# Performance work log

Measured on AMD Instinct MI355X. Metric: run time of the kernel, lower is better.

## Reference

```python
import jax, jax.numpy as jnp
import numpy as np

D_MODEL = 1024
NHEAD = 16
HEAD_DIM = D_MODEL // NHEAD


def setup_inputs() -> dict:
    key = jax.random.key(0)
    ks = jax.random.split(key, 11)
    B, L, D = 4, 2048, D_MODEL
    s = 1.0 / np.sqrt(D)  # ~ torch Linear init scale
    return {
        "queries": jax.random.normal(ks[0], (B, L, D), jnp.float32),
        "keys": jax.random.normal(ks[1], (B, L, D), jnp.float32),
        "values": jax.random.normal(ks[2], (B, L, D), jnp.float32),
        "Wq": jax.random.normal(ks[3], (D, D), jnp.float32) * s,
        "bq": jnp.zeros((D,), jnp.float32),
        "Wk": jax.random.normal(ks[4], (D, D), jnp.float32) * s,
        "bk": jnp.zeros((D,), jnp.float32),
        "Wv": jax.random.normal(ks[5], (D, D), jnp.float32) * s,
        "bv": jnp.zeros((D,), jnp.float32),
        "Wo": jax.random.normal(ks[6], (D, D), jnp.float32) * s,
        "bo": jnp.zeros((D,), jnp.float32),
    }


def reference(queries, keys, values, Wq, bq, Wk, bk, Wv, bv, Wo, bo):
    B, L, D = queries.shape
    H, dh = NHEAD, HEAD_DIM
    # projections (W stored as [in, out])
    q = (queries @ Wq + bq).reshape(B, L, H, dh).transpose(0, 2, 1, 3)  # [B,H,L,dh]
    k = (keys @ Wk + bk).reshape(B, L, H, dh).transpose(0, 2, 1, 3)
    v = (values @ Wv + bv).reshape(B, L, H, dh).transpose(0, 2, 1, 3)
    scores = jnp.einsum("bhqd,bhkd->bhqk", q, k) / jnp.sqrt(jnp.float32(dh))
    attn = jax.nn.softmax(scores, axis=-1)  # dropout p=0 -> identity
    ctx = jnp.einsum("bhqk,bhkd->bhqd", attn, v)
    ctx = ctx.transpose(0, 2, 1, 3).reshape(B, L, D)
    return ctx @ Wo + bo
```

## Files before the change

### kernel.cpp

```cpp
#include <hip/hip_runtime.h>
#include <math.h>


using f32x4 = __attribute__((ext_vector_type(4))) float;
using bf16x8 = __attribute__((ext_vector_type(8))) short;

__device__ __forceinline__ unsigned short f2bf(float x) {
  union { float f; unsigned u; } v; v.f = x;
  unsigned r = v.u + 0x7fff + ((v.u >> 16) & 1);
  return (unsigned short)(r >> 16);
}

__device__ __forceinline__ void g2l16(const void* g, void* l) {
  __builtin_amdgcn_global_load_lds(
      (const __attribute__((address_space(1))) unsigned int*)g,
      (__attribute__((address_space(3))) unsigned int*)l, 16, 0, 0);
}

__global__ __launch_bounds__(256) void wt_k(const float* __restrict__ W,
                                            short* __restrict__ hiT) {
  __shared__ float t[64][65];
  const int n0 = blockIdx.x * 64, k0 = blockIdx.y * 64;
  const int tid = threadIdx.x;
  const int r = tid >> 4, c4 = (tid & 15) * 4;
#pragma unroll
  for (int i = 0; i < 4; i++) {
    const int row = r + i * 16;
    const float4 v = *(const float4*)&W[(size_t)(k0 + row) * 1024 + n0 + c4];
    t[c4 + 0][row] = v.x;
    t[c4 + 1][row] = v.y;
    t[c4 + 2][row] = v.z;
    t[c4 + 3][row] = v.w;
  }
  __syncthreads();
#pragma unroll
  for (int i = 0; i < 4; i++) {
    const int row = r + i * 16;
    short4 h;
    h.x = (short)f2bf(t[row][c4 + 0]);
    h.y = (short)f2bf(t[row][c4 + 1]);
    h.z = (short)f2bf(t[row][c4 + 2]);
    h.w = (short)f2bf(t[row][c4 + 3]);
    *(short4*)&hiT[(size_t)(n0 + row) * 1024 + k0 + c4] = h;
  }
}

template <int AFP32, int EPI>
__global__ __launch_bounds__(256, 2) void gemm_mfma_k(
    const void* __restrict__ A_g, const short* __restrict__ B_g,
    const float* __restrict__ bias, void* __restrict__ out0) {
  __shared__ short smem[64 * 144];
  short* As = smem;
  short* Bs = smem + 4096;

  const int tid = threadIdx.x;
  const int lane = tid & 63;
  const int wave = tid >> 6;
  const int quad = lane >> 4;
  const int l16 = lane & 15;
  const int m0 = blockIdx.x * 128;
  const int n0 = blockIdx.y * 128;
  const int wm = (wave >> 1) * 64;
  const int wn = (wave & 1) * 64;

  const int srow = tid >> 2;
  const int soff = (tid & 3) * 8;
  const int arow = tid >> 1;
  const int acol = (tid & 1) * 16;

  f32x4 acc[4][4];
#pragma unroll
  for (int i = 0; i < 4; i++)
#pragma unroll
    for (int j = 0; j < 4; j++) acc[i][j] = f32x4{0.f, 0.f, 0.f, 0.f};

  float4 apre[4];
  if (AFP32) {
    const float* Af = (const float*)A_g;
#pragma unroll
    for (int j = 0; j < 4; j++)
      apre[j] = *(const float4*)&Af[(size_t)(m0 + arow) * 1024 + acol + j * 4];
  }

  for (int k0 = 0; k0 < 1024; k0 += 32) {
    __syncthreads();
    if (AFP32) {
      short tmp[16];
      const float af[16] = {apre[0].x, apre[0].y, apre[0].z, apre[0].w,
                            apre[1].x, apre[1].y, apre[1].z, apre[1].w,
                            apre[2].x, apre[2].y, apre[2].z, apre[2].w,
                            apre[3].x, apre[3].y, apre[3].z, apre[3].w};
#pragma unroll
      for (int j = 0; j < 16; j++) tmp[j] = (short)f2bf(af[j]);
      *(bf16x8*)&As[arow * 32 + acol] = *(const bf16x8*)&tmp[0];
      *(bf16x8*)&As[arow * 32 + acol + 8] = *(const bf16x8*)&tmp[8];
    } else {
#pragma unroll
      for (int i = 0; i < 2; i++) {
        const int row = srow + i * 64;
        g2l16(&((const short*)A_g)[(size_t)(m0 + row) * 1024 + k0 + soff],
              &As[row * 32 + soff]);
      }
    }
#pragma unroll
    for (int i = 0; i < 2; i++) {
      const int row = srow + i * 64;
      g2l16(&B_g[(size_t)(n0 + row) * 1024 + k0 + soff], &Bs[row * 32 + soff]);
    }
    __syncthreads();

    if (AFP32 && k0 < 992) {
      const float* Af = (const float*)A_g;
#pragma unroll
      for (int j = 0; j < 4; j++)
        apre[j] = *(const float4*)&Af[(size_t)(m0 + arow) * 1024 + k0 + 32 + acol + j * 4];
    }

    bf16x8 ah[4], bh[4];
#pragma unroll
    for (int t = 0; t < 4; t++) {
      ah[t] = *(const bf16x8*)&As[(wm + t * 16 + l16) * 32 + quad * 8];
      bh[t] = *(const bf16x8*)&Bs[(wn + t * 16 + l16) * 32 + quad * 8];
    }
#pragma unroll
    for (int tm = 0; tm < 4; tm++)
#pragma unroll
      for (int tn = 0; tn < 4; tn++)
        acc[tm][tn] = __builtin_amdgcn_mfma_f32_16x16x32_bf16(ah[tm], bh[tn], acc[tm][tn], 0, 0, 0);
  }

  float bz[4];
#pragma unroll
  for (int tn = 0; tn < 4; tn++) bz[tn] = bias[n0 + wn + tn * 16 + l16];

  if (EPI == 2) {
    const int b = m0 >> 11;
    const int lbase = m0 & 2047;
#pragma unroll
    for (int half = 0; half < 2; half++) {
      __syncthreads();
      if ((wave & 1) == half) {
#pragma unroll
        for (int tm = 0; tm < 4; tm++)
#pragma unroll
          for (int tn = 0; tn < 4; tn++)
#pragma unroll
            for (int r = 0; r < 4; r++) {
              const int nl = tn * 16 + l16;
              const int ml = wm + tm * 16 + quad * 4 + r;
              smem[nl * 144 + ml] = (short)f2bf(acc[tm][tn][r] + bz[tn]);
            }
      }
      __syncthreads();
      const int h = (n0 >> 6) + half;
#pragma unroll
      for (int j = 0; j < 4; j++) {
        const int c = tid + j * 256;
        const int d = c >> 4;
        const int mo = (c & 15) * 8;
        *(bf16x8*)&((short*)out0)[((size_t)((b * 16 + h) * 64 + d)) * 2048 + lbase + mo] =
            *(const bf16x8*)&smem[d * 144 + mo];
      }
    }
    return;
  }

#pragma unroll
  for (int tm = 0; tm < 4; tm++) {
#pragma unroll
    for (int tn = 0; tn < 4; tn++) {
      const int n = n0 + wn + tn * 16 + l16;
#pragma unroll
      for (int r = 0; r < 4; r++) {
        const int m = m0 + wm + tm * 16 + quad * 4 + r;
        const float val = acc[tm][tn][r] + bz[tn];
        const int b = m >> 11, lrow = m & 2047;
        const int h = n >> 6, d = n & 63;
        if (EPI == 0) {
          ((short*)out0)[((size_t)(b * 16 + h) * 2048 + lrow) * 64 + d] =
              (short)f2bf(val * 0.125f);
        } else if (EPI == 1) {
          ((short*)out0)[((size_t)(b * 16 + h) * 2048 + lrow) * 64 + d] =
              (short)f2bf(val);
        } else {
          ((float*)out0)[(size_t)m * 1024 + n] = val;
        }
      }
    }
  }
}

__global__ __launch_bounds__(256, 4) void attn3_k(const short* __restrict__ Qp,
                                                  const short* __restrict__ Kp,
                                                  const short* __restrict__ Vt,
                                                  short* __restrict__ Ctx) {
  __shared__ short Ks[64 * 72];
  __shared__ short Vs[64 * 72];
  __shared__ short Ps[128 * 72];

  const int tid = threadIdx.x;
  const int lane = tid & 63;
  const int wave = tid >> 6;
  const int quad = lane >> 4;
  const int l16 = lane & 15;
  const int bh = blockIdx.y;
  const int q0 = blockIdx.x * 128;

  const short* Kb = Kp + (size_t)bh * 2048 * 64;
  const short* Vb = Vt + (size_t)bh * 64 * 2048;

  bf16x8 qf[2][2];
#pragma unroll
  for (int s = 0; s < 2; s++) {
    const short* qp =
        Qp + ((size_t)bh * 2048 + q0 + wave * 32 + s * 16 + l16) * 64 + quad * 8;
    qf[s][0] = *(const bf16x8*)qp;
    qf[s][1] = *(const bf16x8*)(qp + 32);
  }

  bf16x8 ones;
#pragma unroll
  for (int j = 0; j < 8; j++) ones[j] = (short)0x3F80;

  f32x4 O[2][4], lacc[2];
#pragma unroll
  for (int s = 0; s < 2; s++) {
    lacc[s] = f32x4{0.f, 0.f, 0.f, 0.f};
#pragma unroll
    for (int jo = 0; jo < 4; jo++) O[s][jo] = f32x4{0.f, 0.f, 0.f, 0.f};
  }

  const int srow0 = tid >> 3, soff = (tid & 7) * 8;
  const int srow1 = (tid + 256) >> 3;

  bf16x8 kreg[2], vreg[2];
  kreg[0] = *(const bf16x8*)&Kb[(size_t)srow0 * 64 + soff];
  kreg[1] = *(const bf16x8*)&Kb[(size_t)srow1 * 64 + soff];
  vreg[0] = *(const bf16x8*)&Vb[(size_t)srow0 * 2048 + soff];
  vreg[1] = *(const bf16x8*)&Vb[(size_t)srow1 * 2048 + soff];

  for (int kt = 0; kt < 32; kt++) {
    __syncthreads();
    *(bf16x8*)&Ks[srow0 * 72 + soff] = kreg[0];
    *(bf16x8*)&Ks[srow1 * 72 + soff] = kreg[1];
    *(bf16x8*)&Vs[srow0 * 72 + soff] = vreg[0];
    *(bf16x8*)&Vs[srow1 * 72 + soff] = vreg[1];
    __syncthreads();

    if (kt < 31) {
      const int nb = (kt + 1) * 64;
      kreg[0] = *(const bf16x8*)&Kb[(size_t)(nb + srow0) * 64 + soff];
      kreg[1] = *(const bf16x8*)&Kb[(size_t)(nb + srow1) * 64 + soff];
      vreg[0] = *(const bf16x8*)&Vb[(size_t)srow0 * 2048 + nb + soff];
      vreg[1] = *(const bf16x8*)&Vb[(size_t)srow1 * 2048 + nb + soff];
    }

#pragma unroll
    for (int s = 0; s < 2; s++) {
      f32x4 sacc[4];
#pragma unroll
      for (int j = 0; j < 4; j++) sacc[j] = f32x4{0.f, 0.f, 0.f, 0.f};
#pragma unroll
      for (int c = 0; c < 2; c++)
#pragma unroll
        for (int j = 0; j < 4; j++) {
          const bf16x8 kf = *(const bf16x8*)&Ks[(j * 16 + l16) * 72 + c * 32 + quad * 8];
          sacc[j] = __builtin_amdgcn_mfma_f32_16x16x32_bf16(qf[s][c], kf, sacc[j], 0, 0, 0);
        }
#pragma unroll
      for (int j = 0; j < 4; j++)
#pragma unroll
        for (int r = 0; r < 4; r++) {
          const float e = __expf(sacc[j][r]);
          Ps[(wave * 32 + s * 16 + quad * 4 + r) * 72 + j * 16 + l16] =
              (short)(__float_as_uint(e) >> 16);
        }
    }

#pragma unroll
    for (int c = 0; c < 2; c++) {
      const bf16x8 pf0 = *(const bf16x8*)&Ps[(wave * 32 + l16) * 72 + c * 32 + quad * 8];
      const bf16x8 pf1 = *(const bf16x8*)&Ps[(wave * 32 + 16 + l16) * 72 + c * 32 + quad * 8];
      lacc[0] = __builtin_amdgcn_mfma_f32_16x16x32_bf16(pf0, ones, lacc[0], 0, 0, 0);
      lacc[1] = __builtin_amdgcn_mfma_f32_16x16x32_bf16(pf1, ones, lacc[1], 0, 0, 0);
#pragma unroll
      for (int jo = 0; jo < 4; jo++) {
        const bf16x8 vf = *(const bf16x8*)&Vs[(jo * 16 + l16) * 72 + c * 32 + quad * 8];
        O[0][jo] = __builtin_amdgcn_mfma_f32_16x16x32_bf16(pf0, vf, O[0][jo], 0, 0, 0);
        O[1][jo] = __builtin_amdgcn_mfma_f32_16x16x32_bf16(pf1, vf, O[1][jo], 0, 0, 0);
      }
    }
  }

  const int b = bh >> 4, h = bh & 15;
#pragma unroll
  for (int s = 0; s < 2; s++)
#pragma unroll
    for (int r = 0; r < 4; r++) {
      const float inv_l = 1.0f / lacc[s][r];
      const size_t row = (size_t)b * 2048 + q0 + wave * 32 + s * 16 + quad * 4 + r;
#pragma unroll
      for (int jo = 0; jo < 4; jo++)
        Ctx[row * 1024 + h * 64 + jo * 16 + l16] = (short)f2bf(O[s][jo][r] * inv_l);
    }
}

extern "C" void kernel_launch(void* const* d_in, const int* in_sizes, int n_in,
                              void* d_out, int out_size, void* d_ws, size_t ws_size,
                              hipStream_t stream) {
  const float* queries = (const float*)d_in[0];
  const float* keys    = (const float*)d_in[1];
  const float* values  = (const float*)d_in[2];
  const float* Wq = (const float*)d_in[3];
  const float* bq = (const float*)d_in[4];
  const float* Wk = (const float*)d_in[5];
  const float* bk = (const float*)d_in[6];
  const float* Wv = (const float*)d_in[7];
  const float* bv = (const float*)d_in[8];
  const float* Wo = (const float*)d_in[9];
  const float* bo = (const float*)d_in[10];
  float* out = (float*)d_out;

  const size_t PLANE = (size_t)8192 * 1024 * 2;
  const size_t WPL = (size_t)1024 * 1024 * 2;

  char* p = (char*)d_ws;
  short* WqT = (short*)p;  p += WPL;
  short* WkT = (short*)p;  p += WPL;
  short* WvT = (short*)p;  p += WPL;
  short* WoT = (short*)p;  p += WPL;
  short* Qp  = (short*)p;  p += PLANE;
  short* Kp  = (short*)p;  p += PLANE;
  short* Vt  = (short*)p;  p += PLANE;
  short* ctx = (short*)p;  p += PLANE;

  const dim3 blk(256);
  const dim3 wgrid(16, 16);
  wt_k<<<wgrid, blk, 0, stream>>>(Wq, WqT);
  wt_k<<<wgrid, blk, 0, stream>>>(Wk, WkT);
  wt_k<<<wgrid, blk, 0, stream>>>(Wv, WvT);
  wt_k<<<wgrid, blk, 0, stream>>>(Wo, WoT);

  const dim3 ggrid(64, 8);

  gemm_mfma_k<1, 0><<<ggrid, blk, 0, stream>>>(queries, WqT, bq, Qp);
  gemm_mfma_k<1, 1><<<ggrid, blk, 0, stream>>>(keys,    WkT, bk, Kp);
  gemm_mfma_k<1, 2><<<ggrid, blk, 0, stream>>>(values,  WvT, bv, Vt);

  attn3_k<<<dim3(16, 64), blk, 0, stream>>>(Qp, Kp, Vt, ctx);

  gemm_mfma_k<0, 3><<<ggrid, blk, 0, stream>>>(ctx, WoT, bo, out);
}
```

Measured before the change: 407.8 us.

## Batch weight transposes and QKV projections into single launches, coalesce epilogues

Merges the four weight-transpose launches into one 3D-grid kernel and the three QKV projection GEMMs into one kernel indexed by blockIdx.z, so each pass becomes a single launch with more blocks in flight. The Q/K epilogue now stages results through shared memory and writes 16-byte vectors instead of scattered 2-byte stores. The projection kernel raises its launch bounds to 4 blocks per CU, and a dedicated bf16 output-projection kernel is split out. The attention grid is transposed so consecutive blocks cover different heads. The gains depend on launch overhead and store coalescing, while the higher occupancy target risks register spills.

```diff
diff --git a/kernel.cpp b/kernel.cpp
--- a/kernel.cpp
+++ b/kernel.cpp
@@ -17,9 +17,15 @@
       (__attribute__((address_space(3))) unsigned int*)l, 16, 0, 0);
 }
 
-__global__ __launch_bounds__(256) void wt_k(const float* __restrict__ W,
-                                            short* __restrict__ hiT) {
+__global__ __launch_bounds__(256) void wt4_k(const float* __restrict__ W0,
+                                             const float* __restrict__ W1,
+                                             const float* __restrict__ W2,
+                                             const float* __restrict__ W3,
+                                             short* __restrict__ WT) {
   __shared__ float t[64][65];
+  const int z = blockIdx.z;
+  const float* W = z == 0 ? W0 : (z == 1 ? W1 : (z == 2 ? W2 : W3));
+  short* hiT = WT + (size_t)z * 1048576;
   const int n0 = blockIdx.x * 64, k0 = blockIdx.y * 64;
   const int tid = threadIdx.x;
   const int r = tid >> 4, c4 = (tid & 15) * 4;
@@ -45,13 +51,20 @@
   }
 }
 
-template <int AFP32, int EPI>
-__global__ __launch_bounds__(256, 2) void gemm_mfma_k(
-    const void* __restrict__ A_g, const short* __restrict__ B_g,
-    const float* __restrict__ bias, void* __restrict__ out0) {
+__global__ __launch_bounds__(256, 4) void proj3_k(
+    const float* __restrict__ A0, const float* __restrict__ A1,
+    const float* __restrict__ A2, const short* __restrict__ WT,
+    const float* __restrict__ b0, const float* __restrict__ b1,
+    const float* __restrict__ b2, short* __restrict__ Obase) {
   __shared__ short smem[64 * 144];
   short* As = smem;
   short* Bs = smem + 4096;
+
+  const int z = blockIdx.z;
+  const float* A = z == 0 ? A0 : (z == 1 ? A1 : A2);
+  const short* B_g = WT + (size_t)z * 1048576;
+  const float* bias = z == 0 ? b0 : (z == 1 ? b1 : b2);
+  short* outp = Obase + (size_t)z * 8388608;
 
   const int tid = threadIdx.x;
   const int lane = tid & 63;
@@ -75,16 +88,13 @@
     for (int j = 0; j < 4; j++) acc[i][j] = f32x4{0.f, 0.f, 0.f, 0.f};
 
   float4 apre[4];
-  if (AFP32) {
-    const float* Af = (const float*)A_g;
-#pragma unroll
-    for (int j = 0; j < 4; j++)
-      apre[j] = *(const float4*)&Af[(size_t)(m0 + arow) * 1024 + acol + j * 4];
-  }
+#pragma unroll
+  for (int j = 0; j < 4; j++)
+    apre[j] = *(const float4*)&A[(size_t)(m0 + arow) * 1024 + acol + j * 4];
 
   for (int k0 = 0; k0 < 1024; k0 += 32) {
     __syncthreads();
-    if (AFP32) {
+    {
       short tmp[16];
       const float af[16] = {apre[0].x, apre[0].y, apre[0].z, apre[0].w,
                             apre[1].x, apre[1].y, apre[1].z, apre[1].w,
@@ -94,13 +104,6 @@
       for (int j = 0; j < 16; j++) tmp[j] = (short)f2bf(af[j]);
       *(bf16x8*)&As[arow * 32 + acol] = *(const bf16x8*)&tmp[0];
       *(bf16x8*)&As[arow * 32 + acol + 8] = *(const bf16x8*)&tmp[8];
-    } else {
-#pragma unroll
-      for (int i = 0; i < 2; i++) {
-        const int row = srow + i * 64;
-        g2l16(&((const short*)A_g)[(size_t)(m0 + row) * 1024 + k0 + soff],
-              &As[row * 32 + soff]);
-      }
     }
 #pragma unroll
     for (int i = 0; i < 2; i++) {
@@ -109,11 +112,10 @@
     }
     __syncthreads();
 
-    if (AFP32 && k0 < 992) {
-      const float* Af = (const float*)A_g;
+    if (k0 < 992) {
 #pragma unroll
       for (int j = 0; j < 4; j++)
-        apre[j] = *(const float4*)&Af[(size_t)(m0 + arow) * 1024 + k0 + 32 + acol + j * 4];
+        apre[j] = *(const float4*)&A[(size_t)(m0 + arow) * 1024 + k0 + 32 + acol + j * 4];
     }
 
     bf16x8 ah[4], bh[4];
@@ -132,10 +134,12 @@
   float bz[4];
 #pragma unroll
   for (int tn = 0; tn < 4; tn++) bz[tn] = bias[n0 + wn + tn * 16 + l16];
-
-  if (EPI == 2) {
-    const int b = m0 >> 11;
-    const int lbase = m0 & 2047;
+  const float sc = (z == 0) ? 0.125f : 1.0f;
+
+  const int b = m0 >> 11;
+  const int lbase = m0 & 2047;
+
+  if (z == 2) {
 #pragma unroll
     for (int half = 0; half < 2; half++) {
       __syncthreads();
@@ -158,36 +162,102 @@
         const int c = tid + j * 256;
         const int d = c >> 4;
         const int mo = (c & 15) * 8;
-        *(bf16x8*)&((short*)out0)[((size_t)((b * 16 + h) * 64 + d)) * 2048 + lbase + mo] =
+        *(bf16x8*)&outp[((size_t)((b * 16 + h) * 64 + d)) * 2048 + lbase + mo] =
             *(const bf16x8*)&smem[d * 144 + mo];
       }
     }
-    return;
-  }
-
-#pragma unroll
-  for (int tm = 0; tm < 4; tm++) {
+  } else {
+#pragma unroll
+    for (int half = 0; half < 2; half++) {
+      __syncthreads();
+      if ((wave & 1) == half) {
+#pragma unroll
+        for (int tm = 0; tm < 4; tm++)
+#pragma unroll
+          for (int tn = 0; tn < 4; tn++)
+#pragma unroll
+            for (int r = 0; r < 4; r++) {
+              const int ml = wm + tm * 16 + quad * 4 + r;
+              const int nl = tn * 16 + l16;
+              smem[ml * 72 + nl] = (short)f2bf((acc[tm][tn][r] + bz[tn]) * sc);
+            }
+      }
+      __syncthreads();
+      const int h = (n0 >> 6) + half;
+#pragma unroll
+      for (int j = 0; j < 4; j++) {
+        const int c = tid + j * 256;
+        const int ml = c >> 3;
+        const int off = (c & 7) * 8;
+        *(bf16x8*)&outp[((size_t)(b * 16 + h) * 2048 + lbase + ml) * 64 + off] =
+            *(const bf16x8*)&smem[ml * 72 + off];
+      }
+    }
+  }
+}
+
+__global__ __launch_bounds__(256, 2) void outproj_k(
+    const short* __restrict__ A_g, const short* __restrict__ B_g,
+    const float* __restrict__ bias, float* __restrict__ out0) {
+  __shared__ short As[4096];
+  __shared__ short Bs[4096];
+
+  const int tid = threadIdx.x;
+  const int lane = tid & 63;
+  const int wave = tid >> 6;
+  const int quad = lane >> 4;
+  const int l16 = lane & 15;
+  const int m0 = blockIdx.x * 128;
+  const int n0 = blockIdx.y * 128;
+  const int wm = (wave >> 1) * 64;
+  const int wn = (wave & 1) * 64;
+  const int srow = tid >> 2;
+  const int soff = (tid & 3) * 8;
+
+  f32x4 acc[4][4];
+#pragma unroll
+  for (int i = 0; i < 4; i++)
+#pragma unroll
+    for (int j = 0; j < 4; j++) acc[i][j] = f32x4{0.f, 0.f, 0.f, 0.f};
+
+  for (int k0 = 0; k0 < 1024; k0 += 32) {
+    __syncthreads();
+#pragma unroll
+    for (int i = 0; i < 2; i++) {
+      const int row = srow + i * 64;
+      g2l16(&A_g[(size_t)(m0 + row) * 1024 + k0 + soff], &As[row * 32 + soff]);
+      g2l16(&B_g[(size_t)(n0 + row) * 1024 + k0 + soff], &Bs[row * 32 + soff]);
+    }
+    __syncthreads();
+
+    bf16x8 ah[4], bh[4];
+#pragma unroll
+    for (int t = 0; t < 4; t++) {
+      ah[t] = *(const bf16x8*)&As[(wm + t * 16 + l16) * 32 + quad * 8];
+      bh[t] = *(const bf16x8*)&Bs[(wn + t * 16 + l16) * 32 + quad * 8];
+    }
+#pragma unroll
+    for (int tm = 0; tm < 4; tm++)
+#pragma unroll
+      for (int tn = 0; tn < 4; tn++)
+        acc[tm][tn] = __builtin_amdgcn_mfma_f32_16x16x32_bf16(ah[tm], bh[tn], acc[tm][tn], 0, 0, 0);
+  }
+
+  float bz[4];
+#pragma unroll
+  for (int tn = 0; tn < 4; tn++) bz[tn] = bias[n0 + wn + tn * 16 + l16];
+
+#pragma unroll
+  for (int tm = 0; tm < 4; tm++)
 #pragma unroll
     for (int tn = 0; tn < 4; tn++) {
       const int n = n0 + wn + tn * 16 + l16;
 #pragma unroll
       for (int r = 0; r < 4; r++) {
         const int m = m0 + wm + tm * 16 + quad * 4 + r;
-        const float val = acc[tm][tn][r] + bz[tn];
-        const int b = m >> 11, lrow = m & 2047;
-        const int h = n >> 6, d = n & 63;
-        if (EPI == 0) {
-          ((short*)out0)[((size_t)(b * 16 + h) * 2048 + lrow) * 64 + d] =
-              (short)f2bf(val * 0.125f);
-        } else if (EPI == 1) {
-          ((short*)out0)[((size_t)(b * 16 + h) * 2048 + lrow) * 64 + d] =
-              (short)f2bf(val);
-        } else {
-          ((float*)out0)[(size_t)m * 1024 + n] = val;
-        }
-      }
-    }
-  }
+        out0[(size_t)m * 1024 + n] = acc[tm][tn][r] + bz[tn];
+      }
+    }
 }
 
 __global__ __launch_bounds__(256, 4) void attn3_k(const short* __restrict__ Qp,
@@ -203,8 +273,8 @@
   const int wave = tid >> 6;
   const int quad = lane >> 4;
   const int l16 = lane & 15;
-  const int bh = blockIdx.y;
-  const int q0 = blockIdx.x * 128;
+  const int bh = blockIdx.x;
+  const int q0 = blockIdx.y * 128;
 
   const short* Kb = Kp + (size_t)bh * 2048 * 64;
   const short* Vb = Vt + (size_t)bh * 64 * 2048;
@@ -325,29 +395,20 @@
   const size_t WPL = (size_t)1024 * 1024 * 2;
 
   char* p = (char*)d_ws;
-  short* WqT = (short*)p;  p += WPL;
-  short* WkT = (short*)p;  p += WPL;
-  short* WvT = (short*)p;  p += WPL;
-  short* WoT = (short*)p;  p += WPL;
+  short* WT  = (short*)p;  p += 4 * WPL;
   short* Qp  = (short*)p;  p += PLANE;
   short* Kp  = (short*)p;  p += PLANE;
   short* Vt  = (short*)p;  p += PLANE;
   short* ctx = (short*)p;  p += PLANE;
+  (void)Kp;
 
   const dim3 blk(256);
-  const dim3 wgrid(16, 16);
-  wt_k<<<wgrid, blk, 0, stream>>>(Wq, WqT);
-  wt_k<<<wgrid, blk, 0, stream>>>(Wk, WkT);
-  wt_k<<<wgrid, blk, 0, stream>>>(Wv, WvT);
-  wt_k<<<wgrid, blk, 0, stream>>>(Wo, WoT);
-
-  const dim3 ggrid(64, 8);
-
-  gemm_mfma_k<1, 0><<<ggrid, blk, 0, stream>>>(queries, WqT, bq, Qp);
-  gemm_mfma_k<1, 1><<<ggrid, blk, 0, stream>>>(keys,    WkT, bk, Kp);
-  gemm_mfma_k<1, 2><<<ggrid, blk, 0, stream>>>(values,  WvT, bv, Vt);
-
-  attn3_k<<<dim3(16, 64), blk, 0, stream>>>(Qp, Kp, Vt, ctx);
-
-  gemm_mfma_k<0, 3><<<ggrid, blk, 0, stream>>>(ctx, WoT, bo, out);
-}
+  wt4_k<<<dim3(16, 16, 4), blk, 0, stream>>>(Wq, Wk, Wv, Wo, WT);
+
+  proj3_k<<<dim3(64, 8, 3), blk, 0, stream>>>(queries, keys, values, WT,
+                                              bq, bk, bv, Qp);
+
+  attn3_k<<<dim3(64, 16), blk, 0, stream>>>(Qp, Kp, Vt, ctx);
+
+  outproj_k<<<dim3(64, 8), blk, 0, stream>>>(ctx, WT + 3 * 1048576, bo, out);
+}
```

New measurement: 395.9 us. 1.03x faster.
